# Optimization experiments

Hardware: AMD Instinct MI355X
Metric: run time of the kernel (lower is better)

Reference implementation:

```python
import jax, jax.numpy as jnp
from jax import lax
import numpy as np

B, DIM, L_IN = 8, 512, 4096
SCALE = 2
KSIZE = 17
DN = ('NCH', 'OIH', 'NCH')  # conv1d dimension numbers


def _aa_kernel(kernel_size: int, scale: int) -> np.ndarray:
    # replicates scipy.signal.kaiser_atten / kaiser_beta / windows.kaiser
    atten = 2.285 * (kernel_size - 1) * np.pi * (1.0 / scale) + 7.95
    if atten > 50:
        beta = 0.1102 * (atten - 8.7)
    elif atten > 21:
        beta = 0.5842 * (atten - 21) ** 0.4 + 0.07886 * (atten - 21)
    else:
        beta = 0.0
    win = np.kaiser(kernel_size, beta)
    xk = np.arange(kernel_size) - kernel_size // 2
    k = np.sinc(xk / scale) * win  # normalized sinc, same as torch.sinc
    return (k / k.sum()).astype(np.float32)


def setup_inputs() -> dict:
    key = jax.random.key(0)
    k1, k2, k3, k4, k5 = jax.random.split(key, 5)
    kconv = 2 * SCALE - 1
    return {
        'x': jax.random.normal(k1, (B, DIM, L_IN), dtype=jnp.float32),
        'conv_w': jax.random.normal(k2, (DIM, DIM, kconv), dtype=jnp.float32) * (1.0 / np.sqrt(DIM * kconv)),
        'conv_b': jax.random.normal(k3, (DIM,), dtype=jnp.float32) * 0.01,
        'aa_kernel': jnp.asarray(_aa_kernel(KSIZE, SCALE)),
        'proj_w': jax.random.normal(k4, (DIM, DIM), dtype=jnp.float32) * (1.0 / np.sqrt(DIM)),
        'proj_b': jax.random.normal(k5, (DIM,), dtype=jnp.float32) * 0.01,
    }


def reference(x, conv_w, conv_b, aa_kernel, proj_w, proj_b):
    s = SCALE
    # zero-insertion upsample + Conv1d(dim,dim,2s-1,pad=s-1) fused via lhs_dilation.
    # Torch zero-inserts to length l*s (trailing s-1 zeros), so right pad is 2s-2.
    y = lax.conv_general_dilated(
        x, conv_w, window_strides=(1,), padding=[(s - 1, 2 * s - 2)],
        lhs_dilation=(s,), dimension_numbers=DN,
    ) + conv_b[None, :, None]  # [B, D, l*s]
    # depthwise anti-alias filter (same Kaiser-sinc kernel per channel)
    dw = jnp.broadcast_to(aa_kernel, (DIM, 1, KSIZE))
    y = lax.conv_general_dilated(
        y, dw, window_strides=(1,), padding=[(KSIZE // 2, KSIZE // 2)],
        feature_group_count=DIM, dimension_numbers=DN,
    )
    # pointwise 1x1 projection
    return jnp.einsum('bdl,ed->bel', y, proj_w) + proj_b[None, :, None]
```

## Files before the change

### kernel.cpp

```cpp
#include <hip/hip_runtime.h>
#include <hip/hip_bf16.h>

#define BB_   8
#define DIM_  512
#define LIN_  4096
#define LOUT_ 8192

typedef __attribute__((ext_vector_type(8))) __bf16 bf16x8;
typedef __attribute__((ext_vector_type(4))) float  f32x4;
typedef __attribute__((ext_vector_type(8))) unsigned short u16x8;

__device__ __forceinline__ float bf2f(unsigned short u) {
  union { unsigned int i; float f; } x;
  x.i = ((unsigned int)u) << 16;
  return x.f;
}

__device__ __forceinline__ unsigned short f2bf(float f) {
  unsigned int u = __float_as_uint(f);
  return (unsigned short)((u + 0x7fffu + ((u >> 16) & 1u)) >> 16);
}

__device__ __forceinline__ void gload16(const void* g, void* l) {
  __builtin_amdgcn_global_load_lds(
      (__attribute__((address_space(1))) void*)(g),
      (__attribute__((address_space(3))) void*)(l), 16, 0, 0);
}

__global__ __launch_bounds__(256) void k_prep(const float* __restrict__ proj_w,
                                              const float* __restrict__ conv_w,
                                              const float* __restrict__ conv_b,
                                              const float* __restrict__ x,
                                              unsigned short* __restrict__ Mst,
                                              float* __restrict__ Pcb,
                                              unsigned short* __restrict__ Xbt) {
  __shared__ __align__(16) float sm[4160];
  const int bx  = blockIdx.x;
  const int tid = threadIdx.x;

  if (bx < 192) {
    float* Pt = sm;
    float* Wt = sm + 1088;
    const int kk = bx >> 6;
    const int t6 = bx & 63;
    const int et = (t6 >> 3) << 6;
    const int it = (t6 & 7) << 6;
    const int tx = tid & 15, ty = tid >> 4;
    const int le = tid & 63, lg = tid >> 6;
    float acc[4][4] = {};
    for (int d0 = 0; d0 < DIM_; d0 += 16) {
      {
        const float4 v = *(const float4*)&proj_w[(size_t)(et + le) * DIM_ + d0 + lg * 4];
        Pt[(lg * 4 + 0) * 68 + le] = v.x;
        Pt[(lg * 4 + 1) * 68 + le] = v.y;
        Pt[(lg * 4 + 2) * 68 + le] = v.z;
        Pt[(lg * 4 + 3) * 68 + le] = v.w;
      }
#pragma unroll
      for (int r = 0; r < 4; ++r) {
        const int dl = r * 4 + lg;
        Wt[dl * 68 + le] = conv_w[(size_t)(d0 + dl) * (DIM_ * 3) + (it + le) * 3 + kk];
      }
      __syncthreads();
#pragma unroll
      for (int dl = 0; dl < 16; ++dl) {
        const float4 pv = *(const float4*)&Pt[dl * 68 + ty * 4];
        const float4 wv = *(const float4*)&Wt[dl * 68 + tx * 4];
        const float pa[4] = {pv.x, pv.y, pv.z, pv.w};
        const float wa[4] = {wv.x, wv.y, wv.z, wv.w};
#pragma unroll
        for (int a = 0; a < 4; ++a)
#pragma unroll
          for (int b = 0; b < 4; ++b) acc[a][b] += pa[a] * wa[b];
      }
      __syncthreads();
    }
#pragma unroll
    for (int a = 0; a < 4; ++a) {
      uint2 pk;
      pk.x = (unsigned int)f2bf(acc[a][0]) | ((unsigned int)f2bf(acc[a][1]) << 16);
      pk.y = (unsigned int)f2bf(acc[a][2]) | ((unsigned int)f2bf(acc[a][3]) << 16);
      *(uint2*)&Mst[(size_t)(kk * DIM_ + et + ty * 4 + a) * DIM_ + it + tx * 4] = pk;
    }
  } else if (bx < 320) {
    const int idx = bx - 192;
    const int e = idx * 4 + (tid >> 6);
    const int j = tid & 63;
    float s = 0.f;
#pragma unroll
    for (int d = j; d < DIM_; d += 64) s += proj_w[(size_t)e * DIM_ + d] * conv_b[d];
#pragma unroll
    for (int off = 32; off > 0; off >>= 1) s += __shfl_down(s, off, 64);
    if (j == 0) Pcb[e] = s;
  } else {
    const int bc = bx - 320;
    const int bb = bc >> 9;
    const int dt = ((bc >> 6) & 7) << 6;
    const int lt = (bc & 63) << 6;
    const int lr  = tid >> 4;
    const int lc4 = (tid & 15) << 2;
#pragma unroll
    for (int r = 0; r < 4; ++r) {
      const int d = r * 16 + lr;
      const float4 v = *(const float4*)&x[((size_t)(bb * DIM_ + dt + d) << 12) + lt + lc4];
      float* row = sm + d * 65 + lc4;
      row[0] = v.x; row[1] = v.y; row[2] = v.z; row[3] = v.w;
    }
    __syncthreads();
#pragma unroll
    for (int rr = 0; rr < 2; ++rr) {
      const int flat = rr * 256 + tid;
      const int l  = flat >> 3;
      const int d8 = (flat & 7) << 3;
      unsigned int w[4];
#pragma unroll
      for (int p = 0; p < 4; ++p) {
        const float f0 = sm[(d8 + 2 * p + 0) * 65 + l];
        const float f1 = sm[(d8 + 2 * p + 1) * 65 + l];
        w[p] = (unsigned int)f2bf(f0) | ((unsigned int)f2bf(f1) << 16);
      }
      uint4 pk; pk.x = w[0]; pk.y = w[1]; pk.z = w[2]; pk.w = w[3];
      *(uint4*)&Xbt[((size_t)(bb * LIN_ + lt + l) << 9) + dt + d8] = pk;
    }
  }
}

__global__ __launch_bounds__(512, 2) void k_fused(const unsigned short* __restrict__ Xbt,
                                                  const unsigned short* __restrict__ Mst,
                                                  const float* __restrict__ Pcb,
                                                  const float* __restrict__ aa,
                                                  const float* __restrict__ proj_b,
                                                  float* __restrict__ out) {
  __shared__ __align__(16) char lds[131072];
  const int tid = threadIdx.x;
  const int bid = blockIdx.x;
  const int wgs   = (bid & 7) * 128 + (bid >> 3);
  const int ntile = wgs >> 3;
  const int etile = wgs & 7;
  const int bb = ntile >> 4;
  const int L0 = (ntile & 15) << 8;
  const int l0g = L0 - 16;
  const int e0 = etile << 6;

  const int wave = tid >> 6;
  const int lane = tid & 63;

  const unsigned short* src[4];
  int ldso[4];
#pragma unroll
  for (int i = 0; i < 4; ++i) {
    const int u  = wave + 8 * i;
    const int uu = (u >= 30) ? (u - 30) : u;
    const int rl = lane >> 2;
    const int sl = lane & 3;
    int row;
    const unsigned short* p;
    if (uu < 12) {
      row = uu * 16 + rl;
      const int kk = uu >> 2;
      const int er = e0 + ((uu & 3) << 4) + rl;
      p = Mst + ((long long)(kk * 512 + er) << 9);
    } else {
      const int lr = (uu - 12) * 16 + rl;
      row = lr;
      p = Xbt + ((long long)(bb * LIN_) + (l0g + lr)) * 512;
    }
    src[i] = p + ((sl ^ ((row >> 1) & 3)) << 3);
    ldso[i] = u << 10;
  }

#define STAGE_(kt_, buf_)                              \
  do {                                                 \
    char* base_ = lds + (buf_) * 32768;                \
    gload16(src[0] + (kt_) * 32, base_ + ldso[0]);     \
    gload16(src[1] + (kt_) * 32, base_ + ldso[1]);     \
    gload16(src[2] + (kt_) * 32, base_ + ldso[2]);     \
    gload16(src[3] + (kt_) * 32, base_ + ldso[3]);     \
  } while (0)

  const int wm = wave >> 1;
  const int wn = wave & 1;
  const int lrow = lane & 15;
  const int lc   = lane >> 4;
  const int asl  = lc ^ ((lrow >> 1) & 3);
  const char* A0 = lds + ((wm * 48 + lrow) * 64 + asl * 16);
  const char* B0 = lds + (12288 + (wn * 144 + lrow) * 64 + asl * 16);

  f32x4 acc[3][9] = {};

  STAGE_(0, 0); STAGE_(1, 1); STAGE_(2, 2);

#pragma unroll 4
  for (int kt = 0; kt < 16; ++kt) {
    if (kt < 13) {
      STAGE_(kt + 3, (kt + 3) & 3);
      asm volatile("s_waitcnt vmcnt(12)" ::: "memory");
    } else if (kt == 13) {
      asm volatile("s_waitcnt vmcnt(8)" ::: "memory");
    } else if (kt == 14) {
      asm volatile("s_waitcnt vmcnt(4)" ::: "memory");
    } else {
      asm volatile("s_waitcnt vmcnt(0)" ::: "memory");
    }
    __builtin_amdgcn_s_barrier();
    __builtin_amdgcn_sched_barrier(0);

    const int bo = (kt & 3) * 32768;
    bf16x8 af[3], bfv[9];
#pragma unroll
    for (int mt = 0; mt < 3; ++mt) af[mt] = *(const bf16x8*)(A0 + bo + mt * 1024);
#pragma unroll
    for (int nt = 0; nt < 9; ++nt) bfv[nt] = *(const bf16x8*)(B0 + bo + nt * 1024);
#pragma unroll
    for (int mt = 0; mt < 3; ++mt)
#pragma unroll
      for (int nt = 0; nt < 9; ++nt)
        acc[mt][nt] = __builtin_amdgcn_mfma_f32_16x16x32_bf16(bfv[nt], af[mt],
                                                              acc[mt][nt], 0, 0, 0);
    asm volatile("s_waitcnt lgkmcnt(0)" ::: "memory");
    __builtin_amdgcn_sched_barrier(0);
    __builtin_amdgcn_s_barrier();
  }
#undef STAGE_

  unsigned short* Ut = (unsigned short*)lds;
#pragma unroll
  for (int mt = 0; mt < 3; ++mt) {
    const int m = wm * 48 + mt * 16 + lrow;
#pragma unroll
    for (int nt = 0; nt < 9; ++nt) {
      const int lcol = wn * 144 + nt * 16 + (lc << 2);
      uint2 pk;
      pk.x = (unsigned int)f2bf(acc[mt][nt][0]) | ((unsigned int)f2bf(acc[mt][nt][1]) << 16);
      pk.y = (unsigned int)f2bf(acc[mt][nt][2]) | ((unsigned int)f2bf(acc[mt][nt][3]) << 16);
      *(uint2*)&Ut[m * 296 + lcol] = pk;
    }
  }
  __syncthreads();

  const int el  = tid >> 3;
  const int lt0 = (tid & 7) << 5;
  const int e   = e0 + el;
  const float pcb = Pcb[e];
  const float pb  = proj_b[e];
  float sa[17];
#pragma unroll
  for (int j = 0; j < 17; ++j) sa[j] = aa[j];
  const unsigned short* u0r = Ut + (size_t)el * 296;
  const unsigned short* u1r = Ut + (size_t)(64 + el) * 296;
  const unsigned short* u2r = Ut + (size_t)(128 + el) * 296;
  const bool edge = (L0 == 0) || (L0 == 3840);
  float* orow = out + (((size_t)(bb * 512 + e)) << 13) + 2 * (size_t)(L0 + lt0);

#pragma unroll
  for (int cc = 0; cc < 4; ++cc) {
    const int c0 = lt0 + 8 * cc + 12;
    float E[17], O[16];
    if (!edge) {
      const u16x8 e0v = *(const u16x8*)(u1r + c0 - 4);
      const u16x8 e1v = *(const u16x8*)(u1r + c0 + 4);
      const u16x8 e2v = *(const u16x8*)(u1r + c0 + 12);
      const u16x8 a0v = *(const u16x8*)(u0r + c0 - 4);
      const u16x8 a1v = *(const u16x8*)(u0r + c0 + 4);
      const u16x8 a2v = *(const u16x8*)(u0r + c0 + 12);
      const u16x8 b0v = *(const u16x8*)(u2r + c0 - 4);
      const u16x8 b1v = *(const u16x8*)(u2r + c0 + 4);
      const u16x8 b2v = *(const u16x8*)(u2r + c0 + 12);
      unsigned short ue[24], ua[24], ub[24];
#pragma unroll
      for (int j = 0; j < 8; ++j) {
        ue[j] = e0v[j]; ue[j + 8] = e1v[j]; ue[j + 16] = e2v[j];
        ua[j] = a0v[j]; ua[j + 8] = a1v[j]; ua[j + 16] = a2v[j];
        ub[j] = b0v[j]; ub[j + 8] = b1v[j]; ub[j + 16] = b2v[j];
      }
#pragma unroll
      for (int j = 0; j < 17; ++j) E[j] = bf2f(ue[4 + j]) + pcb;
#pragma unroll
      for (int j = 0; j < 16; ++j) O[j] = bf2f(ua[4 + j]) + pcb + bf2f(ub[5 + j]);
    } else {
      const int lt = L0 + lt0 + 8 * cc;
#pragma unroll
      for (int j = 0; j < 17; ++j) {
        const int l = lt - 4 + j;
        E[j] = (l >= 0 && l < 4096) ? (bf2f(u1r[c0 + j]) + pcb) : 0.f;
      }
#pragma unroll
      for (int j = 0; j < 16; ++j) {
        const int l = lt - 4 + j;
        float v = 0.f;
        if (l >= 0 && l < 4096) {
          v = bf2f(u0r[c0 + j]) + pcb;
          if (l + 1 < 4096) v += bf2f(u2r[c0 + j + 1]);
        }
        O[j] = v;
      }
    }
    float res[16];
#pragma unroll
    for (int t = 0; t < 8; ++t) {
      float se = 0.f, so = 0.f;
#pragma unroll
      for (int q = 0; q <= 8; ++q) {
        se += sa[2 * q] * E[t + q];
        so += sa[2 * q] * O[t + q];
      }
#pragma unroll
      for (int q = 0; q < 8; ++q) {
        se += sa[2 * q + 1] * O[t + q];
        so += sa[2 * q + 1] * E[t + q + 1];
      }
      res[2 * t]     = se + pb;
      res[2 * t + 1] = so + pb;
    }
#pragma unroll
    for (int c2 = 0; c2 < 4; ++c2)
      *(float4*)(orow + 16 * cc + 4 * c2) = *(const float4*)&res[4 * c2];
  }
}

extern "C" void kernel_launch(void* const* d_in, const int* in_sizes, int n_in,
                              void* d_out, int out_size, void* d_ws, size_t ws_size,
                              hipStream_t stream) {
  const float* x      = (const float*)d_in[0];
  const float* conv_w = (const float*)d_in[1];
  const float* conv_b = (const float*)d_in[2];
  const float* aa     = (const float*)d_in[3];
  const float* proj_w = (const float*)d_in[4];
  const float* proj_b = (const float*)d_in[5];
  float* out = (float*)d_out;

  char* ws = (char*)d_ws;
  unsigned short* Mst = (unsigned short*)ws;
  float*          Pcb = (float*)(ws + 1572864);
  unsigned short* Xbt = (unsigned short*)(ws + 1574912);

  k_prep<<<dim3(4416, 1, 1), 256, 0, stream>>>(proj_w, conv_w, conv_b, x, Mst, Pcb, Xbt);
  k_fused<<<dim3(1024, 1, 1), 512, 0, stream>>>(Xbt, Mst, Pcb, aa, proj_b, out);
}
```

Baseline: 321.9 us.

## Halve fused-kernel L tile, use triple-buffered pipeline for higher occupancy

Shrinks each workgroup's output length tile from 256 to 128 positions, so the grid doubles to 2048 blocks and the accumulator tile shrinks from 3x9 to 3x5 MFMA fragments. LDS buffering drops from four 32KB stages to three 24KB stages, and launch bounds are raised to four blocks per CU to improve occupancy and latency hiding. Edge handling now clamps X row indices and flags only the boundary segments, and the depthwise epilogue processes one 16-wide segment per thread. In exchange, the 16-row halo is reloaded for more tiles and the prefetch depth is reduced.

After: 328.1 us. Within noise of the previous version (+1.9%).

```diff
diff --git a/kernel.cpp b/kernel.cpp
--- a/kernel.cpp
+++ b/kernel.cpp
@@ -125,57 +125,57 @@
   }
 }
 
-__global__ __launch_bounds__(512, 2) void k_fused(const unsigned short* __restrict__ Xbt,
+__global__ __launch_bounds__(512, 4) void k_fused(const unsigned short* __restrict__ Xbt,
                                                   const unsigned short* __restrict__ Mst,
                                                   const float* __restrict__ Pcb,
                                                   const float* __restrict__ aa,
                                                   const float* __restrict__ proj_b,
                                                   float* __restrict__ out) {
-  __shared__ __align__(16) char lds[131072];
+  __shared__ __align__(16) char lds[73728];
   const int tid = threadIdx.x;
   const int bid = blockIdx.x;
-  const int wgs   = (bid & 7) * 128 + (bid >> 3);
+  const int wgs   = (bid & 7) * 256 + (bid >> 3);
+  const int etile = wgs & 7;
   const int ntile = wgs >> 3;
-  const int etile = wgs & 7;
-  const int bb = ntile >> 4;
-  const int L0 = (ntile & 15) << 8;
+  const int bb = ntile >> 5;
+  const int L0 = (ntile & 31) << 7;
   const int l0g = L0 - 16;
   const int e0 = etile << 6;
 
   const int wave = tid >> 6;
   const int lane = tid & 63;
 
-  const unsigned short* src[4];
-  int ldso[4];
-#pragma unroll
-  for (int i = 0; i < 4; ++i) {
-    const int u  = wave + 8 * i;
-    const int uu = (u >= 30) ? (u - 30) : u;
+  const unsigned short* src[3];
+  int ldso[3];
+  {
     const int rl = lane >> 2;
     const int sl = lane & 3;
-    int row;
-    const unsigned short* p;
-    if (uu < 12) {
-      row = uu * 16 + rl;
-      const int kk = uu >> 2;
-      const int er = e0 + ((uu & 3) << 4) + rl;
-      p = Mst + ((long long)(kk * 512 + er) << 9);
-    } else {
-      const int lr = (uu - 12) * 16 + rl;
-      row = lr;
-      p = Xbt + ((long long)(bb * LIN_) + (l0g + lr)) * 512;
-    }
-    src[i] = p + ((sl ^ ((row >> 1) & 3)) << 3);
-    ldso[i] = u << 10;
+    const int ch = sl ^ ((rl >> 1) & 3);
+#pragma unroll
+    for (int i = 0; i < 3; ++i) {
+      const int u  = wave + 8 * i;
+      const int uu = (u >= 22) ? (u - 22) : u;
+      const unsigned short* p;
+      if (uu < 12) {
+        const int kk = uu >> 2;
+        const int er = e0 + ((uu & 3) << 4) + rl;
+        p = Mst + ((size_t)(kk * 512 + er) << 9);
+      } else {
+        int labs = l0g + (uu - 12) * 16 + rl;
+        labs = labs < 0 ? 0 : (labs > 4095 ? 4095 : labs);
+        p = Xbt + ((size_t)(bb * LIN_ + labs) << 9);
+      }
+      src[i] = p + (ch << 3);
+      ldso[i] = u << 10;
+    }
   }
 
 #define STAGE_(kt_, buf_)                              \
   do {                                                 \
-    char* base_ = lds + (buf_) * 32768;                \
+    char* base_ = lds + (buf_) * 24576;                \
     gload16(src[0] + (kt_) * 32, base_ + ldso[0]);     \
     gload16(src[1] + (kt_) * 32, base_ + ldso[1]);     \
     gload16(src[2] + (kt_) * 32, base_ + ldso[2]);     \
-    gload16(src[3] + (kt_) * 32, base_ + ldso[3]);     \
   } while (0)
 
   const int wm = wave >> 1;
@@ -184,37 +184,35 @@
   const int lc   = lane >> 4;
   const int asl  = lc ^ ((lrow >> 1) & 3);
   const char* A0 = lds + ((wm * 48 + lrow) * 64 + asl * 16);
-  const char* B0 = lds + (12288 + (wn * 144 + lrow) * 64 + asl * 16);
-
-  f32x4 acc[3][9] = {};
-
-  STAGE_(0, 0); STAGE_(1, 1); STAGE_(2, 2);
-
-#pragma unroll 4
+  const char* B0 = lds + (12288 + (wn * 80 + lrow) * 64 + asl * 16);
+
+  f32x4 acc[3][5] = {};
+
+  STAGE_(0, 0); STAGE_(1, 1);
+
+#pragma unroll
   for (int kt = 0; kt < 16; ++kt) {
-    if (kt < 13) {
-      STAGE_(kt + 3, (kt + 3) & 3);
-      asm volatile("s_waitcnt vmcnt(12)" ::: "memory");
-    } else if (kt == 13) {
-      asm volatile("s_waitcnt vmcnt(8)" ::: "memory");
+    if (kt < 14) {
+      STAGE_(kt + 2, (kt + 2) % 3);
+      asm volatile("s_waitcnt vmcnt(6)" ::: "memory");
     } else if (kt == 14) {
-      asm volatile("s_waitcnt vmcnt(4)" ::: "memory");
+      asm volatile("s_waitcnt vmcnt(3)" ::: "memory");
     } else {
       asm volatile("s_waitcnt vmcnt(0)" ::: "memory");
     }
     __builtin_amdgcn_s_barrier();
     __builtin_amdgcn_sched_barrier(0);
 
-    const int bo = (kt & 3) * 32768;
-    bf16x8 af[3], bfv[9];
+    const int bo = (kt % 3) * 24576;
+    bf16x8 af[3], bfv[5];
 #pragma unroll
     for (int mt = 0; mt < 3; ++mt) af[mt] = *(const bf16x8*)(A0 + bo + mt * 1024);
 #pragma unroll
-    for (int nt = 0; nt < 9; ++nt) bfv[nt] = *(const bf16x8*)(B0 + bo + nt * 1024);
+    for (int nt = 0; nt < 5; ++nt) bfv[nt] = *(const bf16x8*)(B0 + bo + nt * 1024);
 #pragma unroll
     for (int mt = 0; mt < 3; ++mt)
 #pragma unroll
-      for (int nt = 0; nt < 9; ++nt)
+      for (int nt = 0; nt < 5; ++nt)
         acc[mt][nt] = __builtin_amdgcn_mfma_f32_16x16x32_bf16(bfv[nt], af[mt],
                                                               acc[mt][nt], 0, 0, 0);
     asm volatile("s_waitcnt lgkmcnt(0)" ::: "memory");
@@ -228,76 +226,74 @@
   for (int mt = 0; mt < 3; ++mt) {
     const int m = wm * 48 + mt * 16 + lrow;
 #pragma unroll
-    for (int nt = 0; nt < 9; ++nt) {
-      const int lcol = wn * 144 + nt * 16 + (lc << 2);
+    for (int nt = 0; nt < 5; ++nt) {
+      const int lcol = wn * 80 + nt * 16 + (lc << 2);
       uint2 pk;
       pk.x = (unsigned int)f2bf(acc[mt][nt][0]) | ((unsigned int)f2bf(acc[mt][nt][1]) << 16);
       pk.y = (unsigned int)f2bf(acc[mt][nt][2]) | ((unsigned int)f2bf(acc[mt][nt][3]) << 16);
-      *(uint2*)&Ut[m * 296 + lcol] = pk;
+      *(uint2*)&Ut[m * 168 + lcol] = pk;
     }
   }
   __syncthreads();
 
   const int el  = tid >> 3;
-  const int lt0 = (tid & 7) << 5;
+  const int seg = tid & 7;
+  const int lt0 = seg << 4;
   const int e   = e0 + el;
   const float pcb = Pcb[e];
   const float pb  = proj_b[e];
   float sa[17];
 #pragma unroll
   for (int j = 0; j < 17; ++j) sa[j] = aa[j];
-  const unsigned short* u0r = Ut + (size_t)el * 296;
-  const unsigned short* u1r = Ut + (size_t)(64 + el) * 296;
-  const unsigned short* u2r = Ut + (size_t)(128 + el) * 296;
-  const bool edge = (L0 == 0) || (L0 == 3840);
-  float* orow = out + (((size_t)(bb * 512 + e)) << 13) + 2 * (size_t)(L0 + lt0);
-
-#pragma unroll
-  for (int cc = 0; cc < 4; ++cc) {
-    const int c0 = lt0 + 8 * cc + 12;
-    float E[17], O[16];
-    if (!edge) {
-      const u16x8 e0v = *(const u16x8*)(u1r + c0 - 4);
-      const u16x8 e1v = *(const u16x8*)(u1r + c0 + 4);
-      const u16x8 e2v = *(const u16x8*)(u1r + c0 + 12);
-      const u16x8 a0v = *(const u16x8*)(u0r + c0 - 4);
-      const u16x8 a1v = *(const u16x8*)(u0r + c0 + 4);
-      const u16x8 a2v = *(const u16x8*)(u0r + c0 + 12);
-      const u16x8 b0v = *(const u16x8*)(u2r + c0 - 4);
-      const u16x8 b1v = *(const u16x8*)(u2r + c0 + 4);
-      const u16x8 b2v = *(const u16x8*)(u2r + c0 + 12);
-      unsigned short ue[24], ua[24], ub[24];
-#pragma unroll
-      for (int j = 0; j < 8; ++j) {
-        ue[j] = e0v[j]; ue[j + 8] = e1v[j]; ue[j + 16] = e2v[j];
-        ua[j] = a0v[j]; ua[j + 8] = a1v[j]; ua[j + 16] = a2v[j];
-        ub[j] = b0v[j]; ub[j + 8] = b1v[j]; ub[j + 16] = b2v[j];
-      }
-#pragma unroll
-      for (int j = 0; j < 17; ++j) E[j] = bf2f(ue[4 + j]) + pcb;
-#pragma unroll
-      for (int j = 0; j < 16; ++j) O[j] = bf2f(ua[4 + j]) + pcb + bf2f(ub[5 + j]);
-    } else {
-      const int lt = L0 + lt0 + 8 * cc;
-#pragma unroll
-      for (int j = 0; j < 17; ++j) {
-        const int l = lt - 4 + j;
-        E[j] = (l >= 0 && l < 4096) ? (bf2f(u1r[c0 + j]) + pcb) : 0.f;
-      }
-#pragma unroll
-      for (int j = 0; j < 16; ++j) {
-        const int l = lt - 4 + j;
-        float v = 0.f;
-        if (l >= 0 && l < 4096) {
-          v = bf2f(u0r[c0 + j]) + pcb;
-          if (l + 1 < 4096) v += bf2f(u2r[c0 + j + 1]);
-        }
-        O[j] = v;
-      }
-    }
-    float res[16];
-#pragma unroll
-    for (int t = 0; t < 8; ++t) {
+  const unsigned short* u0r = Ut + (size_t)el * 168;
+  const unsigned short* u1r = Ut + (size_t)(64 + el) * 168;
+  const unsigned short* u2r = Ut + (size_t)(128 + el) * 168;
+  const int P0 = L0 + lt0;
+  const bool edge = (L0 == 0 && seg == 0) || (L0 == 3968 && seg == 7);
+
+  float E[25], O[24];
+  if (!edge) {
+    u16x8 w1[4], w0[4], w2[4];
+#pragma unroll
+    for (int c = 0; c < 4; ++c) {
+      w1[c] = *(const u16x8*)(u1r + lt0 + 8 + 8 * c);
+      w0[c] = *(const u16x8*)(u0r + lt0 + 8 + 8 * c);
+      w2[c] = *(const u16x8*)(u2r + lt0 + 8 + 8 * c);
+    }
+#pragma unroll
+    for (int j = 0; j < 25; ++j)
+      E[j] = bf2f(w1[(j + 4) >> 3][(j + 4) & 7]) + pcb;
+#pragma unroll
+    for (int j = 0; j < 24; ++j)
+      O[j] = bf2f(w0[(j + 4) >> 3][(j + 4) & 7]) + pcb +
+             bf2f(w2[(j + 5) >> 3][(j + 5) & 7]);
+  } else {
+#pragma unroll
+    for (int j = 0; j < 25; ++j) {
+      const int l = P0 - 4 + j;
+      const int c = lt0 + 12 + j;
+      E[j] = (l >= 0 && l < 4096) ? (bf2f(u1r[c]) + pcb) : 0.f;
+    }
+#pragma unroll
+    for (int j = 0; j < 24; ++j) {
+      const int l = P0 - 4 + j;
+      const int c = lt0 + 12 + j;
+      float v = 0.f;
+      if (l >= 0 && l < 4096) {
+        v = bf2f(u0r[c]) + pcb;
+        if (l + 1 < 4096) v += bf2f(u2r[c + 1]);
+      }
+      O[j] = v;
+    }
+  }
+
+  float* orow = out + (((size_t)(bb * 512 + e)) << 13) + 2 * (size_t)P0;
+#pragma unroll
+  for (int t2 = 0; t2 < 8; ++t2) {
+    float r4[4];
+#pragma unroll
+    for (int h = 0; h < 2; ++h) {
+      const int t = 2 * t2 + h;
       float se = 0.f, so = 0.f;
 #pragma unroll
       for (int q = 0; q <= 8; ++q) {
@@ -309,12 +305,10 @@
         se += sa[2 * q + 1] * O[t + q];
         so += sa[2 * q + 1] * E[t + q + 1];
       }
-      res[2 * t]     = se + pb;
-      res[2 * t + 1] = so + pb;
-    }
-#pragma unroll
-    for (int c2 = 0; c2 < 4; ++c2)
-      *(float4*)(orow + 16 * cc + 4 * c2) = *(const float4*)&res[4 * c2];
+      r4[2 * h]     = se + pb;
+      r4[2 * h + 1] = so + pb;
+    }
+    *(float4*)(orow + 4 * t2) = *(const float4*)r4;
   }
 }
 
@@ -335,5 +329,5 @@
   unsigned short* Xbt = (unsigned short*)(ws + 1574912);
 
   k_prep<<<dim3(4416, 1, 1), 256, 0, stream>>>(proj_w, conv_w, conv_b, x, Mst, Pcb, Xbt);
-  k_fused<<<dim3(1024, 1, 1), 512, 0, stream>>>(Xbt, Mst, Pcb, aa, proj_b, out);
-}
+  k_fused<<<dim3(2048, 1, 1), 512, 0, stream>>>(Xbt, Mst, Pcb, aa, proj_b, out);
+}
```

## Double-buffer LDS fragments, shorten prefetch depth, drop occupancy to one block

Applied to the files above, without the earlier changes.

The main GEMM loop is restructured so the LDS-to-register fragment loads for step kt+1 are issued before the MFMAs of step kt. This overlaps LDS reads with matrix math and removes the trailing lgkmcnt wait and the second barrier per iteration. Global prefetch depth drops from 3 stages to 2, MFMA sections get a raised wave priority via s_setprio, and launch bounds go from 2 blocks per CU to 1 to free registers for the doubled fragments. The X row index is also clamped, which guards out-of-range halo loads. The cost is lower occupancy and less latency hiding for global loads.

Result: no change. 322.0 us (+0.0%).

```diff
diff --git a/kernel.cpp b/kernel.cpp
--- a/kernel.cpp
+++ b/kernel.cpp
@@ -125,7 +125,7 @@
   }
 }
 
-__global__ __launch_bounds__(512, 2) void k_fused(const unsigned short* __restrict__ Xbt,
+__global__ __launch_bounds__(512, 1) void k_fused(const unsigned short* __restrict__ Xbt,
                                                   const unsigned short* __restrict__ Mst,
                                                   const float* __restrict__ Pcb,
                                                   const float* __restrict__ aa,
@@ -147,26 +147,27 @@
 
   const unsigned short* src[4];
   int ldso[4];
-#pragma unroll
-  for (int i = 0; i < 4; ++i) {
-    const int u  = wave + 8 * i;
-    const int uu = (u >= 30) ? (u - 30) : u;
+  {
     const int rl = lane >> 2;
     const int sl = lane & 3;
-    int row;
-    const unsigned short* p;
-    if (uu < 12) {
-      row = uu * 16 + rl;
-      const int kk = uu >> 2;
-      const int er = e0 + ((uu & 3) << 4) + rl;
-      p = Mst + ((long long)(kk * 512 + er) << 9);
-    } else {
-      const int lr = (uu - 12) * 16 + rl;
-      row = lr;
-      p = Xbt + ((long long)(bb * LIN_) + (l0g + lr)) * 512;
-    }
-    src[i] = p + ((sl ^ ((row >> 1) & 3)) << 3);
-    ldso[i] = u << 10;
+    const int ch = sl ^ ((rl >> 1) & 3);
+#pragma unroll
+    for (int i = 0; i < 4; ++i) {
+      const int u  = wave + 8 * i;
+      const int uu = (u >= 30) ? (u - 30) : u;
+      const unsigned short* p;
+      if (uu < 12) {
+        const int kk = uu >> 2;
+        const int er = e0 + ((uu & 3) << 4) + rl;
+        p = Mst + ((size_t)(kk * 512 + er) << 9);
+      } else {
+        int labs = l0g + (uu - 12) * 16 + rl;
+        labs = labs < 0 ? 0 : (labs > 4095 ? 4095 : labs);
+        p = Xbt + ((size_t)(bb * LIN_ + labs) << 9);
+      }
+      src[i] = p + (ch << 3);
+      ldso[i] = u << 10;
+    }
   }
 
 #define STAGE_(kt_, buf_)                              \
@@ -187,17 +188,22 @@
   const char* B0 = lds + (12288 + (wn * 144 + lrow) * 64 + asl * 16);
 
   f32x4 acc[3][9] = {};
-
-  STAGE_(0, 0); STAGE_(1, 1); STAGE_(2, 2);
-
-#pragma unroll 4
+  bf16x8 afr[2][3], bfr[2][9];
+
+  STAGE_(0, 0); STAGE_(1, 1);
+  asm volatile("s_waitcnt vmcnt(4)" ::: "memory");
+  __builtin_amdgcn_s_barrier();
+  __builtin_amdgcn_sched_barrier(0);
+#pragma unroll
+  for (int mt = 0; mt < 3; ++mt) afr[0][mt] = *(const bf16x8*)(A0 + mt * 1024);
+#pragma unroll
+  for (int nt = 0; nt < 9; ++nt) bfr[0][nt] = *(const bf16x8*)(B0 + nt * 1024);
+
+#pragma unroll
   for (int kt = 0; kt < 16; ++kt) {
-    if (kt < 13) {
-      STAGE_(kt + 3, (kt + 3) & 3);
-      asm volatile("s_waitcnt vmcnt(12)" ::: "memory");
-    } else if (kt == 13) {
-      asm volatile("s_waitcnt vmcnt(8)" ::: "memory");
-    } else if (kt == 14) {
+    const int cur = kt & 1, nxt = cur ^ 1;
+    if (kt < 14) {
+      STAGE_(kt + 2, (kt + 2) & 3);
       asm volatile("s_waitcnt vmcnt(4)" ::: "memory");
     } else {
       asm volatile("s_waitcnt vmcnt(0)" ::: "memory");
@@ -205,23 +211,28 @@
     __builtin_amdgcn_s_barrier();
     __builtin_amdgcn_sched_barrier(0);
 
-    const int bo = (kt & 3) * 32768;
-    bf16x8 af[3], bfv[9];
-#pragma unroll
-    for (int mt = 0; mt < 3; ++mt) af[mt] = *(const bf16x8*)(A0 + bo + mt * 1024);
-#pragma unroll
-    for (int nt = 0; nt < 9; ++nt) bfv[nt] = *(const bf16x8*)(B0 + bo + nt * 1024);
+    if (kt < 15) {
+      const int bo = ((kt + 1) & 3) * 32768;
+#pragma unroll
+      for (int mt = 0; mt < 3; ++mt)
+        afr[nxt][mt] = *(const bf16x8*)(A0 + bo + mt * 1024);
+#pragma unroll
+      for (int nt = 0; nt < 9; ++nt)
+        bfr[nxt][nt] = *(const bf16x8*)(B0 + bo + nt * 1024);
+    }
+
+    __builtin_amdgcn_s_setprio(1);
 #pragma unroll
     for (int mt = 0; mt < 3; ++mt)
 #pragma unroll
       for (int nt = 0; nt < 9; ++nt)
-        acc[mt][nt] = __builtin_amdgcn_mfma_f32_16x16x32_bf16(bfv[nt], af[mt],
+        acc[mt][nt] = __builtin_amdgcn_mfma_f32_16x16x32_bf16(bfr[cur][nt],
+                                                              afr[cur][mt],
                                                               acc[mt][nt], 0, 0, 0);
-    asm volatile("s_waitcnt lgkmcnt(0)" ::: "memory");
-    __builtin_amdgcn_sched_barrier(0);
-    __builtin_amdgcn_s_barrier();
+    __builtin_amdgcn_s_setprio(0);
   }
 #undef STAGE_
+  __builtin_amdgcn_s_barrier();
 
   unsigned short* Ut = (unsigned short*)lds;
 #pragma unroll
```
